# Performance work log

Hardware: AMD Instinct MI355X
Metric: run time of the kernel (lower is better)

Reference implementation:

```python
import jax, jax.numpy as jnp
import numpy as np

EPS = 1e-15

def gcn_sparse(x, row, col, ew, W, b, n):
    # PyG GCNConv: h = x@W; add self-loops (weight 1); sym-normalize; aggregate at col (target); + bias
    h = x @ W
    loop = jnp.arange(n)
    r = jnp.concatenate([row, loop])
    c = jnp.concatenate([col, loop])
    w = jnp.concatenate([ew, jnp.ones((n,), x.dtype)])
    deg = jax.ops.segment_sum(w, c, num_segments=n)
    dinv = jnp.where(deg > 0, deg ** -0.5, 0.0)
    norm = dinv[r] * w * dinv[c]
    out = jax.ops.segment_sum(norm[:, None] * h[r], c, num_segments=n)
    return out + b

def gcn_dense(x, adj, W, b):
    # Dense equivalent of dense_to_sparse + GCNConv: existing nonzero self-loops keep their
    # weight, zero-diagonal nodes get a self-loop of weight 1 (add_remaining_self_loops).
    diag = jnp.diagonal(adj)
    adj_h = adj + jnp.diag(jnp.where(diag == 0, 1.0, 0.0).astype(adj.dtype))
    deg = adj_h.sum(axis=0)  # degree at target (col) nodes
    dinv = jnp.where(deg > 0, deg ** -0.5, 0.0)
    a_norm = dinv[:, None] * adj_h * dinv[None, :]  # norm_ij = d_i^-1/2 a_ij d_j^-1/2
    return a_norm.T @ (x @ W) + b  # out_j = sum_i norm_ij h_i

def diff_pool(x, adj, s, mask=None):
    s = jax.nn.softmax(s, axis=-1)
    if mask is not None:
        x = x * mask[:, None]
        s = s * mask[:, None]
    out = s.T @ x                      # [C, F]
    out_adj = s.T @ (adj @ s)          # [C, C]
    link = jnp.linalg.norm(adj - s @ s.T) / adj.size
    ent = jnp.mean(jnp.sum(-s * jnp.log(s + EPS), axis=-1))
    return out, out_adj, link, ent

def setup_inputs() -> dict:
    N, E, F, H, C1, C2, NC = 8192, 262144, 128, 128, 1024, 128, 16
    key = jax.random.key(0)
    ks = jax.random.split(key, 16)
    x0 = jax.random.normal(ks[0], (N, F), dtype=jnp.float32)
    edge_index = jax.random.randint(ks[1], (2, E), 0, N, dtype=jnp.int32)
    edge_weight = jax.random.uniform(ks[2], (E,), dtype=jnp.float32)
    adj = jnp.zeros((N, N), jnp.float32).at[edge_index[0], edge_index[1]].add(edge_weight)
    mask = jnp.ones((N,), jnp.float32)
    g = lambda k, i, o: jax.random.normal(k, (i, o), dtype=jnp.float32) * (1.0 / np.sqrt(i))
    return {
        'x0': x0, 'edge_index': edge_index, 'edge_weight': edge_weight,
        'adj': adj, 'mask': mask,
        'W0_in': g(ks[3], F, H),      'b0_in': jnp.zeros((H,)),
        'Wp1':   g(ks[4], H, C1),     'bp1':   jnp.zeros((C1,)),
        'W1_in': g(ks[5], H, H),      'b1_in': jnp.zeros((H,)),
        'Wp2':   g(ks[6], H, C2),     'bp2':   jnp.zeros((C2,)),
        'W2_in': g(ks[7], H, H),      'b2_in': jnp.zeros((H,)),
        'W1_out': g(ks[8], 2 * H, H), 'b1_out': jnp.zeros((H,)),
        'W0_out': g(ks[9], 2 * H, NC), 'b0_out': jnp.zeros((NC,)),
    }

def reference(x0, edge_index, edge_weight, adj, mask,
              W0_in, b0_in, Wp1, bp1, W1_in, b1_in, Wp2, bp2,
              W2_in, b2_in, W1_out, b1_out, W0_out, b0_out):
    n = x0.shape[0]
    row, col = edge_index[0], edge_index[1]
    x0_ = jax.nn.relu(gcn_sparse(x0, row, col, edge_weight, W0_in, b0_in, n))
    s1 = jax.nn.relu(gcn_sparse(x0_, row, col, edge_weight, Wp1, bp1, n))
    x1, adj1, l1, e1 = diff_pool(x0_, adj, s1, mask)
    x1_ = jax.nn.relu(gcn_dense(x1, adj1, W1_in, b1_in))
    s2 = jax.nn.relu(gcn_dense(x1_, adj1, Wp2, bp2))
    x2, adj2, l2, e2 = diff_pool(x1_, adj1, s2)
    x2_out = jax.nn.relu(gcn_dense(x2, adj2, W2_in, b2_in))
    x2_out_up = s2 @ x2_out  # unpool with pre-softmax relu s2, as in source
    x1_out = jax.nn.relu(gcn_dense(jnp.concatenate([x1_, x2_out_up], axis=1), adj1, W1_out, b1_out))
    x1_out_up = s1 @ x1_out
    x0_out = jax.nn.relu(gcn_sparse(jnp.concatenate([x0_, x1_out_up], axis=1), row, col, edge_weight, W0_out, b0_out, n))
    prediction = jax.nn.log_softmax(x0_out, axis=1)
    edge_loss = l1 + e1 + l2 + e2
    return prediction, s1, edge_loss, adj1
```

## Files before the change

kernel.cpp:

```cpp
#include <hip/hip_runtime.h>
#include <math.h>


#define N_NODES 8192
#define N_EDGES 262144

typedef __attribute__((ext_vector_type(8))) short short8;
typedef __attribute__((ext_vector_type(4))) float floatx4;

#define OFF_DEG     0
#define OFF_CNTC    8192
#define OFF_CNTR    16384
#define OFF_SCAL    24576
#define ZERO_FLOATS 24592
#define OFF_COLPTR  24592
#define OFF_ROWPTR  32785
#define OFF_CURC    40978
#define OFF_CURR    49170
#define OFF_COLR    57362
#define OFF_COLN    319506
#define OFF_ROWC    581650
#define OFF_ROWW    843794
#define OFF_DINV    1105938
#define OFF_X0      1114144
#define OFF_H0      2162720
#define OFF_S       3211296
#define OFF_AN1TB   OFF_S
#define OFF_ADJ1B   (OFF_S+524288)
#define OFF_HAT     (OFF_S+1048576)
#define OFF_HBT     (OFF_S+1114112)
#define OFF_HCATT   (OFF_S+1179648)
#define OFF_S2ST    (OFF_S+1245184)
#define OFF_X0T     7405600
#define OFF_X0B     7929888
#define A2          8454176
#define OFF_X1      (A2+0)
#define OFF_Y16     (A2+131072)
#define OFF_X1_     (A2+262144)
#define OFF_S2      (A2+524288)
#define OFF_S2S     (A2+655360)
#define OFF_U       (A2+786432)
#define OFF_X2      (A2+917504)
#define OFF_ADJ2    (A2+933888)
#define OFF_HC      (A2+950272)
#define OFF_X2_     (A2+966656)
#define OFF_Z2      (A2+999424)
#define OFF_X1O     (A2+1261568)
#define OFF_P16     (A2+1392640)
#define OFF_DEG1    OFF_P16
#define OFF_DIAGV   (OFF_P16+1024)
#define OFF_DI2     (A2+1656832)
#define OFF_DF2     (A2+1656960)
#define OFF_ST      10111264
#define OFF_TBF     14305568
#define OFF_WP1T    OFF_TBF
#define OFF_PT      OFF_TBF
#define OFF_S1B     22694176
#define OFF_TT2     32131360

#define OUT_PRED 0
#define OUT_S1   131072
#define OUT_LOSS 8519680
#define OUT_ADJ1 8519681

__device__ __forceinline__ unsigned short f2bf(float f) {
    union { float f; unsigned u; } v; v.f = f;
    unsigned r = (v.u + 0x7FFF + ((v.u >> 16) & 1)) >> 16;
    return (unsigned short)r;
}
__device__ __forceinline__ float bf2f(unsigned short b) {
    union { unsigned u; float f; } v; v.u = (unsigned)b << 16; return v.f;
}
__device__ __forceinline__ void gl_lds16(const unsigned short* g, unsigned short* l) {
    __builtin_amdgcn_global_load_lds(
        (const __attribute__((address_space(1))) void*)g,
        (__attribute__((address_space(3))) void*)l, 16, 0, 0);
}


__global__ void k_hist(const int* __restrict__ row, const int* __restrict__ col,
                       const float* __restrict__ ew, int E,
                       float* deg, int* cntc, int* cntr, float* sumA2) {
    __shared__ float red[256];
    int e = blockIdx.x * 256 + threadIdx.x;
    float w2 = 0.f;
    if (e < E) {
        int r = row[e], c = col[e];
        float w = ew[e];
        atomicAdd(&deg[c], w);
        atomicAdd(&cntc[c], 1);
        atomicAdd(&cntr[r], 1);
        w2 = w * w;
    }
    red[threadIdx.x] = w2; __syncthreads();
    for (int s = 128; s > 0; s >>= 1) { if (threadIdx.x < s) red[threadIdx.x] += red[threadIdx.x + s]; __syncthreads(); }
    if (threadIdx.x == 0) atomicAdd(sumA2, red[0]);
}

__global__ __launch_bounds__(1024) void k_scan(const int* cntc, const int* cntr,
        int* colptr, int* rowptr, int* curc, int* curr, int n, int E,
        const float* __restrict__ deg, float* __restrict__ dinv) {
    __shared__ int part[1024];
    int tid = threadIdx.x;
    const int per = 8;
    for (int pass = 0; pass < 2; ++pass) {
        const int* cnt = pass ? cntr : cntc;
        int* ptr = pass ? rowptr : colptr;
        int* cur = pass ? curr : curc;
        int st = tid * per;
        int loc[per]; int s = 0;
        for (int i = 0; i < per; ++i) { loc[i] = s; s += cnt[st + i]; }
        part[tid] = s; __syncthreads();
        for (int off = 1; off < 1024; off <<= 1) {
            int v = part[tid];
            int add = (tid >= off) ? part[tid - off] : 0;
            __syncthreads();
            part[tid] = v + add;
            __syncthreads();
        }
// ... 3 lines not shown
        __syncthreads();
    }
    for (int i = tid; i < n; i += 1024) {
        float d = deg[i] + 1.0f;
        dinv[i] = (d > 0.f) ? 1.0f / sqrtf(d) : 0.f;
    }
}

__global__ void k_scatter(const int* __restrict__ row, const int* __restrict__ col,
                          const float* __restrict__ ew, int E, const float* __restrict__ dinv,
                          int* curc, int* curr, int* colr, float* coln, int* rowc, float* roww) {
    int e = blockIdx.x * 256 + threadIdx.x;
    if (e >= E) return;
    int r = row[e], c = col[e];
    float w = ew[e];
    float nrm = dinv[r] * w * dinv[c];
    int p = atomicAdd(&curc[c], 1);
    colr[p] = r; coln[p] = nrm;
    int q = atomicAdd(&curr[r], 1);
    rowc[q] = c; roww[q] = w;
}


__global__ __launch_bounds__(256) void gemm_ab_b16(const float* __restrict__ A, const float* __restrict__ B,
        unsigned short* __restrict__ C, int M, int N, int K) {
    __shared__ float As[16][68];
    __shared__ float Bs[16][68];
    int tid = threadIdx.x, tx = tid & 15, ty = tid >> 4;
    int m0 = blockIdx.y * 64, n0 = blockIdx.x * 64;
    float acc[4][4] = {};
    for (int k0 = 0; k0 < K; k0 += 16) {
        for (int l = 0; l < 4; ++l) {
            int idx = tid + 256 * l;
            int mm = idx >> 4, kk = idx & 15;
            As[kk][mm] = A[(size_t)(m0 + mm) * K + k0 + kk];
            int kk2 = idx >> 6, nn = idx & 63;
            Bs[kk2][nn] = B[(size_t)(k0 + kk2) * N + n0 + nn];
        }
        __syncthreads();
        #pragma unroll
        for (int kk = 0; kk < 16; ++kk) {
            float a[4], b[4];
            #pragma unroll
            for (int i = 0; i < 4; ++i) a[i] = As[kk][ty * 4 + i];
            #pragma unroll
            for (int j = 0; j < 4; ++j) b[j] = Bs[kk][tx * 4 + j];
            #pragma unroll
            for (int i = 0; i < 4; ++i)
                #pragma unroll
                for (int j = 0; j < 4; ++j) acc[i][j] += a[i] * b[j];
        }
        __syncthreads();
    }
    for (int i = 0; i < 4; ++i)
        for (int j = 0; j < 4; ++j)
            C[(size_t)(m0 + ty * 4 + i) * N + n0 + tx * 4 + j] = f2bf(acc[i][j]);
}

__global__ __launch_bounds__(256) void gemm_ab32(const float* __restrict__ A, const float* __restrict__ B,
        float* __restrict__ C, int M, int N, int K,
        const float* __restrict__ bias, int relu, int accum) {
    __shared__ float As[32][33];
    __shared__ float Bs[32][33];
    int tid = threadIdx.x, tx = tid & 15, ty = tid >> 4;
    int m0 = blockIdx.y * 32, n0 = blockIdx.x * 32;
    float acc[2][2] = {};
    for (int k0 = 0; k0 < K; k0 += 32) {
        #pragma unroll
        for (int l = 0; l < 4; ++l) {
            int idx = tid + 256 * l;
            int r = idx >> 5, c = idx & 31;
            As[r][c] = A[(size_t)(m0 + r) * K + k0 + c];
            Bs[r][c] = B[(size_t)(k0 + r) * N + n0 + c];
        }
        __syncthreads();
        #pragma unroll
        for (int kk = 0; kk < 32; ++kk) {
            float a0 = As[ty * 2][kk], a1 = As[ty * 2 + 1][kk];
            float b0 = Bs[kk][tx * 2], b1 = Bs[kk][tx * 2 + 1];
            acc[0][0] += a0 * b0; acc[0][1] += a0 * b1;
            acc[1][0] += a1 * b0; acc[1][1] += a1 * b1;
// ... 215 lines not shown
        #pragma unroll
        for (int i = 0; i < 2; ++i)
            #pragma unroll
            for (int j = 0; j < 2; ++j)
                hC[(size_t)(m0 + ty * 2 + i) * 128 + n0 + tx * 2 + j] = acc[i][j];
    } else {
        if (blockIdx.x | blockIdx.y) return;
        __shared__ float red[256];
        int tid = threadIdx.x;
        float diag = 0.f;
        if (tid < 128) {
            float s = 0.f;
            for (int i = 0; i < 128; ++i) s += adj2[(size_t)i * 128 + tid];
            diag = adj2[(size_t)tid * 128 + tid];
            float fix = (diag == 0.f) ? 1.0f : 0.f;
            s += fix;
            df2[tid] = fix;
            di2[tid] = (s > 0.f) ? 1.0f / sqrtf(s) : 0.f;
        }
        red[tid] = diag; __syncthreads();
        for (int st = 128; st > 0; st >>= 1) { if (tid < st) red[tid] += red[tid + st]; __syncthreads(); }
        if (tid == 0) *cross2_out = red[0];
    }
}

__global__ __launch_bounds__(256) void k_gemm_n16(const float* __restrict__ A, const float* __restrict__ B,
        float* __restrict__ C, int M, int K, int accum) {
    __shared__ float As[16][64];
    __shared__ float Bs[64][16];
    int tid = threadIdx.x;
    int r = tid >> 4, c = tid & 15;
    int m0 = blockIdx.x * 16;
    float acc = 0.f;
    for (int k0 = 0; k0 < K; k0 += 64) {
        #pragma unroll
        for (int l = 0; l < 4; ++l) {
            int idx = tid + 256 * l;
            int rr = idx >> 6, cc = idx & 63;
            As[rr][cc] = A[(size_t)(m0 + rr) * K + k0 + cc];
            int kk = idx >> 4, c2 = idx & 15;
            Bs[kk][c2] = B[(size_t)(k0 + kk) * 16 + c2];
        }
        __syncthreads();
        #pragma unroll 16
        for (int kk = 0; kk < 64; ++kk) acc += As[r][kk] * Bs[kk][c];
        __syncthreads();
    }
    float* p = &C[(size_t)(m0 + r) * 16 + c];
    if (accum) acc += *p;
    *p = acc;
}


__global__ __launch_bounds__(256) void gemm_tn_bf16_tiles(
        const unsigned short* __restrict__ ST_,
        const unsigned short* __restrict__ TT_,
        const unsigned short* __restrict__ X0T_,
        float* __restrict__ P, int K) {
    __shared__ __align__(16) unsigned short As[128 * 64];
    __shared__ __align__(16) unsigned short Bs[128 * 64];
    int tid = threadIdx.x;
    int wave = tid >> 6, lane = tid & 63;
    int wm = wave >> 1, wn = wave & 1;
    int lin = blockIdx.x + gridDim.x * blockIdx.y;
    int p432 = (lin & 7) * 54 + (lin >> 3);
    int f = p432 >> 2, z = p432 & 3;
    int m = 0, Pfx = 0;
    while (f >= Pfx + 17 - m) { Pfx += 17 - m; ++m; }
    int r = f - Pfx;
    int t, n0; const unsigned short* B;
    if (r < 8)           { t = m * 8 + r;                              n0 = r * 128;            B = TT_; }
    else if (r < 16 - m) { int tj = m + (r - 8);
                           t = 64 + (8 * m - m * (m - 1) / 2) + (r - 8); n0 = tj * 128;         B = ST_; }
    else                 { t = 100 + m;                                n0 = 0;                  B = X0T_; }
    int m0 = m * 128;
    int kchunk = K >> 2;
    int k0 = z * kchunk;
    float* Pz = P + ((size_t)z * 108 + t) * 16384;
    floatx4 acc[4][4] = {};
    int q = lane >> 4, lm = lane & 15;
    int lrow = lane >> 3, lcol = (lane & 7) * 8;
    for (int kt = 0; kt < kchunk; kt += 64) {
        int gk0 = k0 + kt;
        #pragma unroll
        for (int p = 0; p < 4; ++p) {
            int rbase = wave * 32 + p * 8;
            int row = rbase + lrow;
            int scol = lcol ^ ((row & 7) * 8);
            gl_lds16(&ST_[(size_t)(m0 + row) * K + gk0 + scol], &As[rbase * 64]);
            gl_lds16(&B[(size_t)(n0 + row) * K + gk0 + scol], &Bs[rbase * 64]);
        }
        __syncthreads();
        #pragma unroll
        for (int ks = 0; ks < 64; ks += 32) {
            short8 af[4], bf[4];
            int kk = ks + q * 8;
            #pragma unroll
            for (int i = 0; i < 4; ++i) {
                int ml = wm * 64 + i * 16 + lm;
                af[i] = *(const short8*)(&As[ml * 64 + (kk ^ ((ml & 7) * 8))]);
                int nl = wn * 64 + i * 16 + lm;
                bf[i] = *(const short8*)(&Bs[nl * 64 + (kk ^ ((nl & 7) * 8))]);
            }
            #pragma unroll
            for (int i = 0; i < 4; ++i)
                #pragma unroll
                for (int j = 0; j < 4; ++j)
                    acc[i][j] = __builtin_amdgcn_mfma_f32_16x16x32_bf16(af[i], bf[j], acc[i][j], 0, 0, 0);
        }
        __syncthreads();
    }
    for (int i = 0; i < 4; ++i) {
        int lr = wm * 64 + i * 16 + q * 4;
// ... 64 lines not shown
    if (kind == 0) {
        atomicAdd(&colsum[cc + 0], cs0);
        atomicAdd(&colsum[cc + 1], cs1);
        atomicAdd(&colsum[cc + 2], cs2);
        atomicAdd(&colsum[cc + 3], cs3);
    }
    __syncthreads();
    if (kind == 0 && tid < 128)
        atomicAdd(&deg1[n * 128 + tid], colsum[tid]);
    red[tid] = ss; __syncthreads();
    for (int s = 128; s > 0; s >>= 1) { if (tid < s) red[tid] += red[tid + s]; __syncthreads(); }
    if (tid == 0) atomicAdd((kind == 0) ? &scal[4] : &scal[2], red[0]);
    if (diagTile) {
        __syncthreads();
        red[tid] = tr; __syncthreads();
        for (int s = 128; s > 0; s >>= 1) { if (tid < s) red[tid] += red[tid + s]; __syncthreads(); }
        if (tid == 0) atomicAdd(&scal[1], red[0]);
    }
}

__global__ __launch_bounds__(256) void gemm_tn_bf16_n128(
        const unsigned short* __restrict__ A, const unsigned short* __restrict__ B,
        float* __restrict__ C, int K,
        const float* __restrict__ bias, int relu) {
    __shared__ __align__(16) unsigned short As[64 * 64];
    __shared__ __align__(16) unsigned short Bs[64 * 64];
    int tid = threadIdx.x, wave = tid >> 6, lane = tid & 63;
    int m0 = blockIdx.x * 64, n0 = blockIdx.y * 64;
    floatx4 acc[4] = {};
    int q = lane >> 4, lm = lane & 15;
    int lrow = lane >> 3, lcol = (lane & 7) * 8;
    for (int kt = 0; kt < K; kt += 64) {
        #pragma unroll
        for (int p = 0; p < 2; ++p) {
            int rbase = wave * 16 + p * 8;
            int row = rbase + lrow;
            int scol = lcol ^ ((row & 7) * 8);
            gl_lds16(&A[(size_t)(m0 + row) * K + kt + scol], &As[rbase * 64]);
            gl_lds16(&B[(size_t)(n0 + row) * K + kt + scol], &Bs[rbase * 64]);
        }
        __syncthreads();
        #pragma unroll
        for (int ks = 0; ks < 64; ks += 32) {
            int kk = ks + q * 8;
            int ml = wave * 16 + lm;
            short8 af = *(const short8*)(&As[ml * 64 + (kk ^ ((ml & 7) * 8))]);
            #pragma unroll
            for (int j = 0; j < 4; ++j) {
                int nl = j * 16 + lm;
                short8 bf = *(const short8*)(&Bs[nl * 64 + (kk ^ ((nl & 7) * 8))]);
                acc[j] = __builtin_amdgcn_mfma_f32_16x16x32_bf16(af, bf, acc[j], 0, 0, 0);
            }
        }
        __syncthreads();
    }
    #pragma unroll
    for (int j = 0; j < 4; ++j) {
        int col = n0 + j * 16 + lm;
        float bv = bias ? bias[col] : 0.f;
        int rowb = m0 + wave * 16 + q * 4;
        #pragma unroll
        for (int r = 0; r < 4; ++r) {
            float v = acc[j][r] + bv;
            if (relu) v = fmaxf(v, 0.f);
            C[(size_t)(rowb + r) * 128 + col] = v;
        }
    }
}

__global__ __launch_bounds__(256) void gemm_tn_bf16_store(
        const unsigned short* __restrict__ A, const unsigned short* __restrict__ B,
        float* __restrict__ C, unsigned short* __restrict__ Cb, int M, int N, int K,
        const float* __restrict__ bias, int relu) {
    __shared__ __align__(16) unsigned short As[128 * 64];
    __shared__ __align__(16) unsigned short Bs[128 * 64];
    int tid = threadIdx.x;
    int wave = tid >> 6, lane = tid & 63;
    int wm = wave >> 1, wn = wave & 1;
    int m0 = blockIdx.x * 128, n0 = blockIdx.y * 128;
    floatx4 acc[4][4] = {};
    int q = lane >> 4, lm = lane & 15;
    int lrow = lane >> 3, lcol = (lane & 7) * 8;
    for (int kt = 0; kt < K; kt += 64) {
        #pragma unroll
        for (int p = 0; p < 4; ++p) {
            int rbase = wave * 32 + p * 8;
            int row = rbase + lrow;
            int scol = lcol ^ ((row & 7) * 8);
            gl_lds16(&A[(size_t)(m0 + row) * K + kt + scol], &As[rbase * 64]);
// ... 69 lines not shown
            for (int ks = 0; ks < 64; ks += 32) {
                int kk = ks + q * 8;
                short8 bf = *(const short8*)(&Bs[lm * 64 + (kk ^ ((lm & 7) * 8))]);
                #pragma unroll
                for (int i = 0; i < 2; ++i) {
                    int ml = wave * 32 + i * 16 + lm;
                    short8 af = *(const short8*)(&As[ml * 64 + (kk ^ ((ml & 7) * 8))]);
                    acc[i] = __builtin_amdgcn_mfma_f32_16x16x32_bf16(af, bf, acc[i], 0, 0, 0);
                }
            }
            __syncthreads();
        }
    }
    #pragma unroll
    for (int i = 0; i < 2; ++i) {
        int rowb = m0 + wave * 32 + i * 16 + q * 4;
        #pragma unroll
        for (int r = 0; r < 4; ++r)
            C[(size_t)(rowb + r) * 16 + lm] = acc[i][r];
    }
}


__global__ __launch_bounds__(256) void k_transpose_f2b(
        const float* __restrict__ in, unsigned short* __restrict__ outb,
        int R, int C, const float* __restrict__ rowscale) {
    __shared__ float tile[64][65];
    int rb = blockIdx.y * 64, cb = blockIdx.x * 64;
    int t = threadIdx.x;
    int lr = t >> 4, lc4 = (t & 15) * 4;
    #pragma unroll
    for (int p = 0; p < 4; ++p) {
        int r = rb + lr + p * 16;
        float4 v = *(const float4*)(in + (size_t)r * C + cb + lc4);
        float s = rowscale ? rowscale[r] : 1.0f;
        tile[lr + p * 16][lc4 + 0] = v.x * s;
        tile[lr + p * 16][lc4 + 1] = v.y * s;
        tile[lr + p * 16][lc4 + 2] = v.z * s;
        tile[lr + p * 16][lc4 + 3] = v.w * s;
    }
    __syncthreads();
    int cc0 = t >> 5, rr = (t & 31) * 2;
    #pragma unroll
    for (int p = 0; p < 8; ++p) {
        int cc = cc0 + p * 8;
        unsigned a = f2bf(tile[rr][cc]);
        unsigned b = f2bf(tile[rr + 1][cc]);
        *(unsigned*)(outb + (size_t)(cb + cc) * R + rb + rr) = a | (b << 16);
    }
}

__global__ __launch_bounds__(256) void k_transpose_b2b2(
        const unsigned short* __restrict__ in0, unsigned short* __restrict__ out0,
        const unsigned short* __restrict__ in1, unsigned short* __restrict__ out1,
        int R, int C) {
    __shared__ __align__(16) unsigned short tile[64][72];
    const unsigned short* in = blockIdx.z ? in1 : in0;
    unsigned short* out = blockIdx.z ? out1 : out0;
    int rb = blockIdx.y * 64, cb = blockIdx.x * 64;
    int t = threadIdx.x;
    int lr = t >> 3, lc = (t & 7) * 8;
    #pragma unroll
    for (int p = 0; p < 2; ++p) {
        int r = lr + p * 32;
        *(short8*)(&tile[r][lc]) = *(const short8*)(&in[(size_t)(rb + r) * C + cb + lc]);
    }
    __syncthreads();
    int cc0 = t >> 4, rr = (t & 15) * 4;
    #pragma unroll
    for (int p = 0; p < 4; ++p) {
        int cc = cc0 + p * 16;
        unsigned long long v = (unsigned long long)tile[rr][cc]
                             | ((unsigned long long)tile[rr + 1][cc] << 16)
                             | ((unsigned long long)tile[rr + 2][cc] << 32)
                             | ((unsigned long long)tile[rr + 3][cc] << 48);
        *(unsigned long long*)(&out[(size_t)(cb + cc) * R + rb + rr]) = v;
    }
}

__global__ __launch_bounds__(256) void k_anorm_tb(const float* __restrict__ adjm, int n,
        const float* __restrict__ deg1, const float* __restrict__ diagv,
        unsigned short* __restrict__ outb) {
    __shared__ float tile[64][65];
    __shared__ float drow[64], frow[64], dcol[64];
    int rb = blockIdx.y * 64, cb = blockIdx.x * 64;
    int t = threadIdx.x;
    if (t < 64) {
        int i = rb + t;
        float fi = (diagv[i] == 0.f) ? 1.0f : 0.f;
        float s = deg1[i] + fi;
        frow[t] = fi;
        drow[t] = (s > 0.f) ? 1.0f / sqrtf(s) : 0.f;
    } else if (t < 128) {
        int j = cb + (t - 64);
        float fj = (diagv[j] == 0.f) ? 1.0f : 0.f;
        float s = deg1[j] + fj;
        dcol[t - 64] = (s > 0.f) ? 1.0f / sqrtf(s) : 0.f;
    }
    __syncthreads();
    int lr = t >> 4, lc4 = (t & 15) * 4;
    #pragma unroll
    for (int p = 0; p < 4; ++p) {
        int rl = lr + p * 16;
        int i = rb + rl;
        float4 v = *(const float4*)(adjm + (size_t)i * n + cb + lc4);
        float di = drow[rl];
        float vv[4] = {v.x, v.y, v.z, v.w};
        #pragma unroll
        for (int qq = 0; qq < 4; ++qq) {
            int j = cb + lc4 + qq;
            float val = vv[qq];
            if (i == j) val += frow[rl];
            tile[rl][lc4 + qq] = di * val * dcol[lc4 + qq];
        }
    }
    __syncthreads();
    int cc0 = t >> 5, rr = (t & 31) * 2;
    #pragma unroll
    for (int p = 0; p < 8; ++p) {
        int cc = cc0 + p * 8;
        unsigned a = f2bf(tile[rr][cc]);
        unsigned b = f2bf(tile[rr + 1][cc]);
        *(unsigned*)(outb + (size_t)(cb + cc) * n + rb + rr) = a | (b << 16);
    }
}


__global__ __launch_bounds__(64) void k_agg_b16(const unsigned short* __restrict__ h,
        float* __restrict__ out, unsigned short* __restrict__ outb,
        const int* __restrict__ cptr, const int* __restrict__ colr,
        const float* __restrict__ coln, const float* __restrict__ dinv,
        const float* __restrict__ bias, int relu) {
    int c = blockIdx.x, t = threadIdx.x;
    int f0 = t * 2;
    float d = dinv[c], dd = d * d;
    const unsigned short* hf = h + f0;
    unsigned u = *(const unsigned*)(hf + (size_t)c * 128);
    float a0 = dd * bf2f((unsigned short)(u & 0xffff));
    float a1 = dd * bf2f((unsigned short)(u >> 16));
    int e0 = cptr[c], e1 = cptr[c + 1];
    int e = e0;
    for (; e + 4 <= e1; e += 4) {
        int r0 = colr[e], r1 = colr[e + 1], r2 = colr[e + 2], r3 = colr[e + 3];
        float w0 = coln[e], w1 = coln[e + 1], w2 = coln[e + 2], w3 = coln[e + 3];
        unsigned v0 = *(const unsigned*)(hf + (size_t)r0 * 128);
        unsigned v1 = *(const unsigned*)(hf + (size_t)r1 * 128);
        unsigned v2 = *(const unsigned*)(hf + (size_t)r2 * 128);
// ... 102 lines not shown
    float v = xr[tid];
    red[tid] = v; __syncthreads();
    for (int s = 64; s > 0; s >>= 1) { if (tid < s) red[tid] = fmaxf(red[tid], red[tid + s]); __syncthreads(); }
    float m = red[0]; __syncthreads();
    float e = expf(v - m);
    red[tid] = e; __syncthreads();
    for (int s = 64; s > 0; s >>= 1) { if (tid < s) red[tid] += red[tid + s]; __syncthreads(); }
    float Z = red[0];
    float inv = 1.0f / Z, lz = logf(Z);
    __syncthreads();
    float sv = e * inv;
    S[(size_t)row * 128 + tid] = sv;
    STb[(size_t)tid * 1024 + row] = f2bf(sv);
    red[tid] = sv * (m + lz - v); __syncthreads();
    for (int s = 64; s > 0; s >>= 1) { if (tid < s) red[tid] += red[tid + s]; __syncthreads(); }
    if (tid == 0) atomicAdd(ent_acc, red[0]);
}

__global__ __launch_bounds__(256) void k_spmm_seg(const unsigned short* __restrict__ Sb,
        const int* __restrict__ rptr, const int* __restrict__ rowc, const float* __restrict__ roww,
        unsigned short* __restrict__ tb) {
    int wave = threadIdx.x >> 6, lane = threadIdx.x & 63;
    int r = blockIdx.x * 4 + wave;
    int j0 = blockIdx.y * 256 + lane * 4;
    const unsigned short* Sj = Sb + j0;
    float a0 = 0.f, a1 = 0.f, a2 = 0.f, a3 = 0.f;
    int e0 = rptr[r], e1 = rptr[r + 1];
    int e = e0;
    for (; e + 4 <= e1; e += 4) {
        int c0 = rowc[e], c1 = rowc[e + 1], c2 = rowc[e + 2], c3 = rowc[e + 3];
        float w0 = roww[e], w1 = roww[e + 1], w2 = roww[e + 2], w3 = roww[e + 3];
        uint2 v0 = *(const uint2*)(Sj + (size_t)c0 * 1024);
        uint2 v1 = *(const uint2*)(Sj + (size_t)c1 * 1024);
        uint2 v2 = *(const uint2*)(Sj + (size_t)c2 * 1024);
        uint2 v3 = *(const uint2*)(Sj + (size_t)c3 * 1024);
        a0 += w0 * bf2f((unsigned short)(v0.x & 0xffff)) + w1 * bf2f((unsigned short)(v1.x & 0xffff))
            + w2 * bf2f((unsigned short)(v2.x & 0xffff)) + w3 * bf2f((unsigned short)(v3.x & 0xffff));
        a1 += w0 * bf2f((unsigned short)(v0.x >> 16)) + w1 * bf2f((unsigned short)(v1.x >> 16))
            + w2 * bf2f((unsigned short)(v2.x >> 16)) + w3 * bf2f((unsigned short)(v3.x >> 16));
        a2 += w0 * bf2f((unsigned short)(v0.y & 0xffff)) + w1 * bf2f((unsigned short)(v1.y & 0xffff))
            + w2 * bf2f((unsigned short)(v2.y & 0xffff)) + w3 * bf2f((unsigned short)(v3.y & 0xffff));
        a3 += w0 * bf2f((unsigned short)(v0.y >> 16)) + w1 * bf2f((unsigned short)(v1.y >> 16))
            + w2 * bf2f((unsigned short)(v2.y >> 16)) + w3 * bf2f((unsigned short)(v3.y >> 16));
    }
    for (; e < e1; ++e) {
        int c = rowc[e]; float w = roww[e];
        uint2 v = *(const uint2*)(Sj + (size_t)c * 1024);
        a0 += w * bf2f((unsigned short)(v.x & 0xffff));
        a1 += w * bf2f((unsigned short)(v.x >> 16));
        a2 += w * bf2f((unsigned short)(v.y & 0xffff));
        a3 += w * bf2f((unsigned short)(v.y >> 16));
    }
    unsigned lo = (unsigned)f2bf(a0) | ((unsigned)f2bf(a1) << 16);
    unsigned hi = (unsigned)f2bf(a2) | ((unsigned)f2bf(a3) << 16);
    unsigned long long o = (unsigned long long)lo | ((unsigned long long)hi << 32);
    *(unsigned long long*)(tb + (size_t)r * 1024 + j0) = o;
}


extern "C" void kernel_launch(void* const* d_in, const int* in_sizes, int n_in,
                              void* d_out, int out_size, void* d_ws, size_t ws_size,
                              hipStream_t stream) {
    const int N = N_NODES, E = N_EDGES;
    const float* x0     = (const float*)d_in[0];
    const int*   eidx   = (const int*)d_in[1];
    const float* ew     = (const float*)d_in[2];
    const float* mask   = (const float*)d_in[4];
    const float* W0_in  = (const float*)d_in[5];
    const float* b0_in  = (const float*)d_in[6];
    const float* Wp1    = (const float*)d_in[7];
    const float* bp1    = (const float*)d_in[8];
    const float* W1_in  = (const float*)d_in[9];
    const float* b1_in  = (const float*)d_in[10];
    const float* Wp2    = (const float*)d_in[11];
    const float* bp2    = (const float*)d_in[12];
    const float* W2_in  = (const float*)d_in[13];
    const float* b2_in  = (const float*)d_in[14];
    const float* W1_out = (const float*)d_in[15];
    const float* b1_out = (const float*)d_in[16];
// ... 29 lines not shown
    unsigned short* ADJ1B = (unsigned short*)(wsf + OFF_ADJ1B);
    unsigned short* HAT   = (unsigned short*)(wsf + OFF_HAT);
    unsigned short* HBT   = (unsigned short*)(wsf + OFF_HBT);
    unsigned short* HCATT = (unsigned short*)(wsf + OFF_HCATT);
    unsigned short* S2ST  = (unsigned short*)(wsf + OFF_S2ST);
    unsigned short* ST    = (unsigned short*)(wsf + OFF_ST);
    unsigned short* TBF   = (unsigned short*)(wsf + OFF_TBF);
    unsigned short* WP1T  = (unsigned short*)(wsf + OFF_WP1T);
    unsigned short* X0T   = (unsigned short*)(wsf + OFF_X0T);
    unsigned short* x0b   = (unsigned short*)(wsf + OFF_X0B);
    unsigned short* s1b   = (unsigned short*)(wsf + OFF_S1B);
    float* PT    = wsf + OFF_PT;
    float* x1    = wsf + OFF_X1;
    float* y16   = wsf + OFF_Y16;
    float* x1_   = wsf + OFF_X1_;
    float* s2    = wsf + OFF_S2;
    float* S2s   = wsf + OFF_S2S;
    float* u     = wsf + OFF_U;
    float* x2    = wsf + OFF_X2;
    float* adj2  = wsf + OFF_ADJ2;
    float* hC    = wsf + OFF_HC;
    float* x2_   = wsf + OFF_X2_;
    float* z2    = wsf + OFF_Z2;
    float* x1o_  = wsf + OFF_X1O;
    float* p16   = wsf + OFF_P16;
    float* deg1  = wsf + OFF_DEG1;
    float* diagv = wsf + OFF_DIAGV;
    float* di2   = wsf + OFF_DI2;
    float* df2   = wsf + OFF_DF2;

    const int* row = eidx;
    const int* col = eidx + E;

    hipMemsetAsync(wsf, 0, (size_t)ZERO_FLOATS * sizeof(float), stream);
    hipMemsetAsync(deg1, 0, 1024 * sizeof(float), stream);

    k_hist<<<E / 256, 256, 0, stream>>>(row, col, ew, E, deg, cntc, cntr, &scal[3]);
    k_scan<<<1, 1024, 0, stream>>>(cntc, cntr, cptr, rptr, curc, curr, N, E, deg, dinv);
    k_scatter<<<E / 256, 256, 0, stream>>>(row, col, ew, E, dinv, curc, curr, colr, coln, rowc, roww);

    gemm_ab_b16<<<dim3(2, 128), 256, 0, stream>>>(x0, W0_in, h0b, 8192, 128, 128);
    k_agg_b16<<<N, 64, 0, stream>>>(h0b, x0_, x0b, cptr, colr, coln, dinv, b0_in, 1);

    k_agg_b16<<<N, 64, 0, stream>>>(x0b, nullptr, h0b, cptr, colr, coln, dinv, nullptr, 0);
    k_transpose_f2b<<<dim3(16, 2), 256, 0, stream>>>(Wp1, WP1T, 128, 1024, nullptr);
    gemm_tn_bf16_store<<<dim3(64, 8), 256, 0, stream>>>(h0b, WP1T, s1o, s1b, 8192, 1024, 128, bp1, 1);

    k_softmax1024<<<N, 256, 0, stream>>>(s1o, Sb, mask, &scal[0]);
    k_spmm_seg<<<dim3(N / 4, 4), 256, 0, stream>>>(Sb, rptr, rowc, roww, TBF);
    k_transpose_b2b2<<<dim3(16, 128, 2), 256, 0, stream>>>(Sb, ST, TBF, TT, 8192, 1024);
    k_transpose_f2b<<<dim3(2, 128), 256, 0, stream>>>(x0_, X0T, 8192, 128, mask);

    gemm_tn_bf16_tiles<<<dim3(108, 4), 256, 0, stream>>>(ST, TT, X0T, PT, 8192);
    k_reduce_tiles<<<dim3(2, 108), 256, 0, stream>>>(PT, adj1o, ADJ1B, x1, deg1, diagv, scal);
    k_anorm_tb<<<dim3(16, 16), 256, 0, stream>>>(adj1o, 1024, deg1, diagv, AN1TB);

    gemm_ab32_bt<<<dim3(4, 32), 256, 0, stream>>>(x1, W1_in, HAT, 1024, 128, 128);
    gemm_tn_bf16_n128<<<dim3(16, 2), 256, 0, stream>>>(AN1TB, HAT, x1_, 1024, b1_in, 1);
    gemm_ab32_bt<<<dim3(4, 32), 256, 0, stream>>>(x1_, Wp2, HBT, 1024, 128, 128);
    gemm_tn_bf16_n128<<<dim3(16, 2), 256, 0, stream>>>(AN1TB, HBT, s2, 1024, bp2, 1);

    k_softmax128_t<<<1024, 128, 0, stream>>>(s2, S2s, S2ST, &scal[5]);
    gemm_tn_bf16_n128<<<dim3(16, 2), 256, 0, stream>>>(ADJ1B, S2ST, u, 1024, nullptr, 0);
    k_atb32_3<<<dim3(4, 4, 3), 256, 0, stream>>>(S2s, x1_, u, S2s, x2, adj2, &scal[7], 128, 128, 1024);

    k_hC_coldfix<<<dim3(4, 4, 2), 256, 0, stream>>>(x2, W2_in, hC, adj2, di2, df2, &scal[6]);
    gemm_atb32n<<<dim3(4, 4), 256, 0, stream>>>(adj2, hC, x2_, 128, 128, 128, b2_in, di2, df2, di2);

    gemm_ab32<<<dim3(4, 4), 256, 0, stream>>>(x2_, W1_out + 128 * 128, z2, 128, 128, 128, nullptr, 0, 0);
    gemm_dual_bt<<<dim3(4, 32), 256, 0, stream>>>(x1_, W1_out, s2, z2, HCATT, 1024, 128, 128);
    gemm_tn_bf16_n128<<<dim3(16, 2), 256, 0, stream>>>(AN1TB, HCATT, x1o_, 1024, b1_out, 1);

    k_gemm_n16<<<64, 256, 0, stream>>>(x1o_, W0_out + 128 * 16, y16, 1024, 128, 0);
    k_gemm16_mfma<<<64, 256, 0, stream>>>(x0b, s1b, W0_out, y16, p16);
    k_agg16_ls<<<512, 256, 0, stream>>>(p16, predo, cptr, colr, coln, dinv, b0_out, scal, losso);
}
```

Baseline: 883.9 us.

## Merge independent small kernels and fuse the x1_out projection into its GEMM epilogue

```diff
diff --git a/kernel.cpp b/kernel.cpp
--- a/kernel.cpp
+++ b/kernel.cpp
@@ -45,7 +45,6 @@
 #define OFF_HC      (A2+950272)
 #define OFF_X2_     (A2+966656)
 #define OFF_Z2      (A2+999424)
-#define OFF_X1O     (A2+1261568)
 #define OFF_P16     (A2+1392640)
 #define OFF_DEG1    OFF_P16
 #define OFF_DIAGV   (OFF_P16+1024)
@@ -78,23 +77,64 @@
 }
 
 
-__global__ void k_hist(const int* __restrict__ row, const int* __restrict__ col,
-                       const float* __restrict__ ew, int E,
-                       float* deg, int* cntc, int* cntr, float* sumA2) {
-    __shared__ float red[256];
-    int e = blockIdx.x * 256 + threadIdx.x;
-    float w2 = 0.f;
-    if (e < E) {
-        int r = row[e], c = col[e];
-        float w = ew[e];
-        atomicAdd(&deg[c], w);
-        atomicAdd(&cntc[c], 1);
-        atomicAdd(&cntr[r], 1);
-        w2 = w * w;
-    }
-    red[threadIdx.x] = w2; __syncthreads();
-    for (int s = 128; s > 0; s >>= 1) { if (threadIdx.x < s) red[threadIdx.x] += red[threadIdx.x + s]; __syncthreads(); }
-    if (threadIdx.x == 0) atomicAdd(sumA2, red[0]);
+__global__ __launch_bounds__(256) void k_hist_gemm(
+        const int* __restrict__ row, const int* __restrict__ col,
+        const float* __restrict__ ew, int E,
+        float* deg, int* cntc, int* cntr, float* sumA2,
+        const float* __restrict__ A, const float* __restrict__ B,
+        unsigned short* __restrict__ C) {
+    __shared__ float As[16][68];
+    __shared__ float Bs[16][68];
+    int tid = threadIdx.x;
+    if (blockIdx.x < 1024) {
+        float* red = &As[0][0];
+        int e = blockIdx.x * 256 + tid;
+        float w2 = 0.f;
+        if (e < E) {
+            int r = row[e], c = col[e];
+            float w = ew[e];
+            atomicAdd(&deg[c], w);
+            atomicAdd(&cntc[c], 1);
+            atomicAdd(&cntr[r], 1);
+            w2 = w * w;
+        }
+        red[tid] = w2; __syncthreads();
+        for (int s = 128; s > 0; s >>= 1) { if (tid < s) red[tid] += red[tid + s]; __syncthreads(); }
+        if (tid == 0) atomicAdd(sumA2, red[0]);
+        return;
+    }
+    int bidx = blockIdx.x - 1024;
+    int tx = tid & 15, ty = tid >> 4;
+    int m0 = (bidx >> 1) * 64, n0 = (bidx & 1) * 64;
+    const int M = 8192, N = 128, K = 128;
+    float acc[4][4] = {};
+    for (int k0 = 0; k0 < K; k0 += 16) {
+        for (int l = 0; l < 4; ++l) {
+            int idx = tid + 256 * l;
+            int mm = idx >> 4, kk = idx & 15;
+            As[kk][mm] = A[(size_t)(m0 + mm) * K + k0 + kk];
+            int kk2 = idx >> 6, nn = idx & 63;
+            Bs[kk2][nn] = B[(size_t)(k0 + kk2) * N + n0 + nn];
+        }
+        __syncthreads();
+        #pragma unroll
+        for (int kk = 0; kk < 16; ++kk) {
+            float a[4], b[4];
+            #pragma unroll
+            for (int i = 0; i < 4; ++i) a[i] = As[kk][ty * 4 + i];
+            #pragma unroll
+            for (int j = 0; j < 4; ++j) b[j] = Bs[kk][tx * 4 + j];
+            #pragma unroll
+            for (int i = 0; i < 4; ++i)
+                #pragma unroll
+                for (int j = 0; j < 4; ++j) acc[i][j] += a[i] * b[j];
+        }
+        __syncthreads();
+    }
+    for (int i = 0; i < 4; ++i)
+        for (int j = 0; j < 4; ++j)
+            C[(size_t)(m0 + ty * 4 + i) * N + n0 + tx * 4 + j] = f2bf(acc[i][j]);
+    (void)M;
 }
 
 __global__ __launch_bounds__(1024) void k_scan(const int* cntc, const int* cntr,
@@ -144,41 +184,6 @@
 }
 
 
-__global__ __launch_bounds__(256) void gemm_ab_b16(const float* __restrict__ A, const float* __restrict__ B,
-        unsigned short* __restrict__ C, int M, int N, int K) {
-    __shared__ float As[16][68];
-    __shared__ float Bs[16][68];
-    int tid = threadIdx.x, tx = tid & 15, ty = tid >> 4;
-    int m0 = blockIdx.y * 64, n0 = blockIdx.x * 64;
-    float acc[4][4] = {};
-    for (int k0 = 0; k0 < K; k0 += 16) {
-        for (int l = 0; l < 4; ++l) {
-            int idx = tid + 256 * l;
-            int mm = idx >> 4, kk = idx & 15;
-            As[kk][mm] = A[(size_t)(m0 + mm) * K + k0 + kk];
-            int kk2 = idx >> 6, nn = idx & 63;
-            Bs[kk2][nn] = B[(size_t)(k0 + kk2) * N + n0 + nn];
-        }
-        __syncthreads();
-        #pragma unroll
-        for (int kk = 0; kk < 16; ++kk) {
-            float a[4], b[4];
-            #pragma unroll
-            for (int i = 0; i < 4; ++i) a[i] = As[kk][ty * 4 + i];
-            #pragma unroll
-            for (int j = 0; j < 4; ++j) b[j] = Bs[kk][tx * 4 + j];
-            #pragma unroll
-            for (int i = 0; i < 4; ++i)
-                #pragma unroll
-                for (int j = 0; j < 4; ++j) acc[i][j] += a[i] * b[j];
-        }
-        __syncthreads();
-    }
-    for (int i = 0; i < 4; ++i)
-        for (int j = 0; j < 4; ++j)
-            C[(size_t)(m0 + ty * 4 + i) * N + n0 + tx * 4 + j] = f2bf(acc[i][j]);
-}
-
 __global__ __launch_bounds__(256) void gemm_ab32(const float* __restrict__ A, const float* __restrict__ B,
         float* __restrict__ C, int M, int N, int K,
         const float* __restrict__ bias, int relu, int accum) {
@@ -440,33 +445,6 @@
         for (int st = 128; st > 0; st >>= 1) { if (tid < st) red[tid] += red[tid + st]; __syncthreads(); }
         if (tid == 0) *cross2_out = red[0];
     }
-}
-
-__global__ __launch_bounds__(256) void k_gemm_n16(const float* __restrict__ A, const float* __restrict__ B,
-        float* __restrict__ C, int M, int K, int accum) {
-    __shared__ float As[16][64];
-    __shared__ float Bs[64][16];
-    int tid = threadIdx.x;
-    int r = tid >> 4, c = tid & 15;
-    int m0 = blockIdx.x * 16;
-    float acc = 0.f;
-    for (int k0 = 0; k0 < K; k0 += 64) {
-        #pragma unroll
-        for (int l = 0; l < 4; ++l) {
-            int idx = tid + 256 * l;
-            int rr = idx >> 6, cc = idx & 63;
-            As[rr][cc] = A[(size_t)(m0 + rr) * K + k0 + cc];
-            int kk = idx >> 4, c2 = idx & 15;
-            Bs[kk][c2] = B[(size_t)(k0 + kk) * 16 + c2];
-        }
-        __syncthreads();
-        #pragma unroll 16
-        for (int kk = 0; kk < 64; ++kk) acc += As[r][kk] * Bs[kk][c];
-        __syncthreads();
-    }
-    float* p = &C[(size_t)(m0 + r) * 16 + c];
-    if (accum) acc += *p;
-    *p = acc;
 }
 
 
@@ -487,10 +465,10 @@
     while (f >= Pfx + 17 - m) { Pfx += 17 - m; ++m; }
     int r = f - Pfx;
     int t, n0; const unsigned short* B;
-    if (r < 8)           { t = m * 8 + r;                              n0 = r * 128;            B = TT_; }
+    if (r < 8)           { t = m * 8 + r;                                n0 = r * 128;    B = TT_; }
     else if (r < 16 - m) { int tj = m + (r - 8);
-                           t = 64 + (8 * m - m * (m - 1) / 2) + (r - 8); n0 = tj * 128;         B = ST_; }
-    else                 { t = 100 + m;                                n0 = 0;                  B = X0T_; }
+                           t = 64 + (8 * m - m * (m - 1) / 2) + (r - 8); n0 = tj * 128;   B = ST_; }
+    else                 { t = 100 + m;                                  n0 = 0;          B = X0T_; }
     int m0 = m * 128;
     int kchunk = K >> 2;
     int k0 = z * kchunk;
@@ -503,10 +481,10 @@
         #pragma unroll
         for (int p = 0; p < 4; ++p) {
             int rbase = wave * 32 + p * 8;
-            int row = rbase + lrow;
-            int scol = lcol ^ ((row & 7) * 8);
-            gl_lds16(&ST_[(size_t)(m0 + row) * K + gk0 + scol], &As[rbase * 64]);
-            gl_lds16(&B[(size_t)(n0 + row) * K + gk0 + scol], &Bs[rbase * 64]);
+            int rrow = rbase + lrow;
+            int scol = lcol ^ ((rrow & 7) * 8);
+            gl_lds16(&ST_[(size_t)(m0 + rrow) * K + gk0 + scol], &As[rbase * 64]);
+            gl_lds16(&B[(size_t)(n0 + rrow) * K + gk0 + scol], &Bs[rbase * 64]);
         }
         __syncthreads();
         #pragma unroll
@@ -617,9 +595,11 @@
 __global__ __launch_bounds__(256) void gemm_tn_bf16_n128(
         const unsigned short* __restrict__ A, const unsigned short* __restrict__ B,
         float* __restrict__ C, int K,
-        const float* __restrict__ bias, int relu) {
+        const float* __restrict__ bias, int relu,
+        const float* __restrict__ Wy, float* __restrict__ y16acc) {
     __shared__ __align__(16) unsigned short As[64 * 64];
     __shared__ __align__(16) unsigned short Bs[64 * 64];
+    __shared__ float Cs[64 * 65];
     int tid = threadIdx.x, wave = tid >> 6, lane = tid & 63;
     int m0 = blockIdx.x * 64, n0 = blockIdx.y * 64;
     floatx4 acc[4] = {};
@@ -651,15 +631,32 @@
     }
     #pragma unroll
     for (int j = 0; j < 4; ++j) {
-        int col = n0 + j * 16 + lm;
+        int lc = j * 16 + lm;
+        int col = n0 + lc;
         float bv = bias ? bias[col] : 0.f;
-        int rowb = m0 + wave * 16 + q * 4;
+        int lrb = wave * 16 + q * 4;
         #pragma unroll
         for (int r = 0; r < 4; ++r) {
             float v = acc[j][r] + bv;
             if (relu) v = fmaxf(v, 0.f);
-            C[(size_t)(rowb + r) * 128 + col] = v;
-        }
+            if (C) C[(size_t)(m0 + lrb + r) * 128 + col] = v;
+            if (Wy) Cs[(lrb + r) * 65 + lc] = v;
+        }
+    }
+    if (!Wy) return;
+    float* Wys = (float*)Bs;
+    for (int e = tid; e < 1024; e += 256)
+        Wys[e] = Wy[(size_t)(n0 + (e >> 4)) * 16 + (e & 15)];
+    __syncthreads();
+    #pragma unroll
+    for (int k4 = 0; k4 < 4; ++k4) {
+        int oidx = tid * 4 + k4;
+        int orow = oidx >> 4, ocol = oidx & 15;
+        float val = 0.f;
+        #pragma unroll 16
+        for (int j = 0; j < 64; ++j)
+            val += Cs[orow * 65 + j] * Wys[j * 16 + ocol];
+        atomicAdd(&y16acc[(size_t)(m0 + orow) * 16 + ocol], val);
     }
 }
 
@@ -775,32 +772,40 @@
 }
 
 
-__global__ __launch_bounds__(256) void k_transpose_f2b(
+__device__ __forceinline__ void f2b_body(float* tile ,
         const float* __restrict__ in, unsigned short* __restrict__ outb,
-        int R, int C, const float* __restrict__ rowscale) {
-    __shared__ float tile[64][65];
-    int rb = blockIdx.y * 64, cb = blockIdx.x * 64;
-    int t = threadIdx.x;
+        int R, int C, const float* __restrict__ rowscale, int bx, int by, int t) {
+    int rb = by * 64, cb = bx * 64;
     int lr = t >> 4, lc4 = (t & 15) * 4;
     #pragma unroll
     for (int p = 0; p < 4; ++p) {
         int r = rb + lr + p * 16;
         float4 v = *(const float4*)(in + (size_t)r * C + cb + lc4);
         float s = rowscale ? rowscale[r] : 1.0f;
-        tile[lr + p * 16][lc4 + 0] = v.x * s;
-        tile[lr + p * 16][lc4 + 1] = v.y * s;
-        tile[lr + p * 16][lc4 + 2] = v.z * s;
-        tile[lr + p * 16][lc4 + 3] = v.w * s;
+        tile[(lr + p * 16) * 65 + lc4 + 0] = v.x * s;
+        tile[(lr + p * 16) * 65 + lc4 + 1] = v.y * s;
+        tile[(lr + p * 16) * 65 + lc4 + 2] = v.z * s;
+        tile[(lr + p * 16) * 65 + lc4 + 3] = v.w * s;
     }
     __syncthreads();
     int cc0 = t >> 5, rr = (t & 31) * 2;
     #pragma unroll
     for (int p = 0; p < 8; ++p) {
         int cc = cc0 + p * 8;
-        unsigned a = f2bf(tile[rr][cc]);
-        unsigned b = f2bf(tile[rr + 1][cc]);
+        unsigned a = f2bf(tile[rr * 65 + cc]);
+        unsigned b = f2bf(tile[(rr + 1) * 65 + cc]);
         *(unsigned*)(outb + (size_t)(cb + cc) * R + rb + rr) = a | (b << 16);
     }
+}
+
+__global__ __launch_bounds__(256) void k_f2b2(
+        const float* __restrict__ in0, unsigned short* __restrict__ out0,
+        const float* __restrict__ in1, unsigned short* __restrict__ out1,
+        const float* __restrict__ mask) {
+    __shared__ float tile[64 * 65];
+    int b = blockIdx.x, t = threadIdx.x;
+    if (b < 32) f2b_body(tile, in0, out0, 128, 1024, nullptr, b & 15, b >> 4, t);
+    else { int bb = b - 32; f2b_body(tile, in1, out1, 8192, 128, mask, bb & 1, bb >> 1, t); }
 }
 
 __global__ __launch_bounds__(256) void k_transpose_b2b2(
@@ -831,51 +836,98 @@
     }
 }
 
-__global__ __launch_bounds__(256) void k_anorm_tb(const float* __restrict__ adjm, int n,
+__global__ __launch_bounds__(256) void k_anorm_hat(const float* __restrict__ adjm,
         const float* __restrict__ deg1, const float* __restrict__ diagv,
-        unsigned short* __restrict__ outb) {
-    __shared__ float tile[64][65];
-    __shared__ float drow[64], frow[64], dcol[64];
-    int rb = blockIdx.y * 64, cb = blockIdx.x * 64;
+        unsigned short* __restrict__ outb,
+        const float* __restrict__ Ax1, const float* __restrict__ BW1,
+        unsigned short* __restrict__ HATo) {
+    __shared__ float sm[64 * 65 + 192];
     int t = threadIdx.x;
-    if (t < 64) {
-        int i = rb + t;
-        float fi = (diagv[i] == 0.f) ? 1.0f : 0.f;
-        float s = deg1[i] + fi;
-        frow[t] = fi;
-        drow[t] = (s > 0.f) ? 1.0f / sqrtf(s) : 0.f;
-    } else if (t < 128) {
-        int j = cb + (t - 64);
-        float fj = (diagv[j] == 0.f) ? 1.0f : 0.f;
-        float s = deg1[j] + fj;
-        dcol[t - 64] = (s > 0.f) ? 1.0f / sqrtf(s) : 0.f;
-    }
+    if (blockIdx.x < 256) {
+        const int n = 1024;
+        float* tile = sm;
+        float* drow = sm + 4160;
+        float* frow = sm + 4224;
+        float* dcol = sm + 4288;
+        int rb = (blockIdx.x >> 4) * 64, cb = (blockIdx.x & 15) * 64;
+        if (t < 64) {
+            int i = rb + t;
+            float fi = (diagv[i] == 0.f) ? 1.0f : 0.f;
+            float s = deg1[i] + fi;
+            frow[t] = fi;
+            drow[t] = (s > 0.f) ? 1.0f / sqrtf(s) : 0.f;
+        } else if (t < 128) {
+            int j = cb + (t - 64);
+            float fj = (diagv[j] == 0.f) ? 1.0f : 0.f;
+            float s = deg1[j] + fj;
+            dcol[t - 64] = (s > 0.f) ? 1.0f / sqrtf(s) : 0.f;
+        }
+        __syncthreads();
+        int lr = t >> 4, lc4 = (t & 15) * 4;
+        #pragma unroll
+        for (int p = 0; p < 4; ++p) {
+            int rl = lr + p * 16;
+            int i = rb + rl;
+            float4 v = *(const float4*)(adjm + (size_t)i * n + cb + lc4);
+            float di = drow[rl];
+            float vv[4] = {v.x, v.y, v.z, v.w};
+            #pragma unroll
+            for (int qq = 0; qq < 4; ++qq) {
+                int j = cb + lc4 + qq;
+                float val = vv[qq];
+                if (i == j) val += frow[rl];
+                tile[rl * 65 + lc4 + qq] = di * val * dcol[lc4 + qq];
+            }
+        }
+        __syncthreads();
+        int cc0 = t >> 5, rr = (t & 31) * 2;
+        #pragma unroll
+        for (int p = 0; p < 8; ++p) {
+            int cc = cc0 + p * 8;
+            unsigned a = f2bf(tile[rr * 65 + cc]);
+            unsigned b = f2bf(tile[(rr + 1) * 65 + cc]);
+            *(unsigned*)(outb + (size_t)(cb + cc) * n + rb + rr) = a | (b << 16);
+        }
+        return;
+    }
+    int bb = blockIdx.x - 256;
+    float* As = sm;
+    float* Bs = sm + 1056;
+    int tx = t & 15, ty = t >> 4;
+    int m0 = (bb >> 2) * 32, n0 = (bb & 3) * 32;
+    const int M = 1024, N = 128, K = 128;
+    float acc[2][2] = {};
+    for (int k0 = 0; k0 < K; k0 += 32) {
+        #pragma unroll
+        for (int l = 0; l < 4; ++l) {
+            int idx = t + 256 * l;
+            int r = idx >> 5, c = idx & 31;
+            As[r * 33 + c] = Ax1[(size_t)(m0 + r) * K + k0 + c];
+            Bs[r * 33 + c] = BW1[(size_t)(k0 + r) * N + n0 + c];
+        }
+        __syncthreads();
+        #pragma unroll
+        for (int kk = 0; kk < 32; ++kk) {
+            float a0 = As[(ty * 2) * 33 + kk], a1 = As[(ty * 2 + 1) * 33 + kk];
+            float b0 = Bs[kk * 33 + tx * 2], b1 = Bs[kk * 33 + tx * 2 + 1];
+            acc[0][0] += a0 * b0; acc[0][1] += a0 * b1;
+            acc[1][0] += a1 * b0; acc[1][1] += a1 * b1;
+        }
+        __syncthreads();
+    }
+    #pragma unroll
+    for (int i = 0; i < 2; ++i)
+        #pragma unroll
+        for (int j = 0; j < 2; ++j)
+            As[(ty * 2 + i) * 33 + tx * 2 + j] = acc[i][j];
     __syncthreads();
-    int lr = t >> 4, lc4 = (t & 15) * 4;
-    #pragma unroll
-    for (int p = 0; p < 4; ++p) {
-        int rl = lr + p * 16;
-        int i = rb + rl;
-        float4 v = *(const float4*)(adjm + (size_t)i * n + cb + lc4);
-        float di = drow[rl];
-        float vv[4] = {v.x, v.y, v.z, v.w};
-        #pragma unroll
-        for (int qq = 0; qq < 4; ++qq) {
-            int j = cb + lc4 + qq;
-            float val = vv[qq];
-            if (i == j) val += frow[rl];
-            tile[rl][lc4 + qq] = di * val * dcol[lc4 + qq];
-        }
-    }
-    __syncthreads();
-    int cc0 = t >> 5, rr = (t & 31) * 2;
-    #pragma unroll
-    for (int p = 0; p < 8; ++p) {
-        int cc = cc0 + p * 8;
-        unsigned a = f2bf(tile[rr][cc]);
-        unsigned b = f2bf(tile[rr + 1][cc]);
-        *(unsigned*)(outb + (size_t)(cb + cc) * n + rb + rr) = a | (b << 16);
-    }
+    int nl = t >> 3, moff = (t & 7) * 4;
+    ushort4 o;
+    o.x = f2bf(As[(moff + 0) * 33 + nl]);
+    o.y = f2bf(As[(moff + 1) * 33 + nl]);
+    o.z = f2bf(As[(moff + 2) * 33 + nl]);
+    o.w = f2bf(As[(moff + 3) * 33 + nl]);
+    *(ushort4*)(HATo + (size_t)(n0 + nl) * M + m0 + moff) = o;
 }
 
 
@@ -1024,39 +1076,29 @@
         unsigned short* __restrict__ tb) {
     int wave = threadIdx.x >> 6, lane = threadIdx.x & 63;
     int r = blockIdx.x * 4 + wave;
-    int j0 = blockIdx.y * 256 + lane * 4;
+    int j0 = lane * 16;
     const unsigned short* Sj = Sb + j0;
-    float a0 = 0.f, a1 = 0.f, a2 = 0.f, a3 = 0.f;
+    float a[16] = {};
     int e0 = rptr[r], e1 = rptr[r + 1];
-    int e = e0;
-    for (; e + 4 <= e1; e += 4) {
-        int c0 = rowc[e], c1 = rowc[e + 1], c2 = rowc[e + 2], c3 = rowc[e + 3];
-        float w0 = roww[e], w1 = roww[e + 1], w2 = roww[e + 2], w3 = roww[e + 3];
-        uint2 v0 = *(const uint2*)(Sj + (size_t)c0 * 1024);
-        uint2 v1 = *(const uint2*)(Sj + (size_t)c1 * 1024);
-        uint2 v2 = *(const uint2*)(Sj + (size_t)c2 * 1024);
-        uint2 v3 = *(const uint2*)(Sj + (size_t)c3 * 1024);
-        a0 += w0 * bf2f((unsigned short)(v0.x & 0xffff)) + w1 * bf2f((unsigned short)(v1.x & 0xffff))
-            + w2 * bf2f((unsigned short)(v2.x & 0xffff)) + w3 * bf2f((unsigned short)(v3.x & 0xffff));
-        a1 += w0 * bf2f((unsigned short)(v0.x >> 16)) + w1 * bf2f((unsigned short)(v1.x >> 16))
-            + w2 * bf2f((unsigned short)(v2.x >> 16)) + w3 * bf2f((unsigned short)(v3.x >> 16));
-        a2 += w0 * bf2f((unsigned short)(v0.y & 0xffff)) + w1 * bf2f((unsigned short)(v1.y & 0xffff))
-            + w2 * bf2f((unsigned short)(v2.y & 0xffff)) + w3 * bf2f((unsigned short)(v3.y & 0xffff));
-        a3 += w0 * bf2f((unsigned short)(v0.y >> 16)) + w1 * bf2f((unsigned short)(v1.y >> 16))
-            + w2 * bf2f((unsigned short)(v2.y >> 16)) + w3 * bf2f((unsigned short)(v3.y >> 16));
-    }
-    for (; e < e1; ++e) {
+    for (int e = e0; e < e1; ++e) {
         int c = rowc[e]; float w = roww[e];
-        uint2 v = *(const uint2*)(Sj + (size_t)c * 1024);
-        a0 += w * bf2f((unsigned short)(v.x & 0xffff));
-        a1 += w * bf2f((unsigned short)(v.x >> 16));
-        a2 += w * bf2f((unsigned short)(v.y & 0xffff));
-        a3 += w * bf2f((unsigned short)(v.y >> 16));
-    }
-    unsigned lo = (unsigned)f2bf(a0) | ((unsigned)f2bf(a1) << 16);
-    unsigned hi = (unsigned)f2bf(a2) | ((unsigned)f2bf(a3) << 16);
-    unsigned long long o = (unsigned long long)lo | ((unsigned long long)hi << 32);
-    *(unsigned long long*)(tb + (size_t)r * 1024 + j0) = o;
+        const unsigned short* p = Sj + (size_t)c * 1024;
+        uint4 v0 = *(const uint4*)(p);
+        uint4 v1 = *(const uint4*)(p + 8);
+        unsigned vv[8] = {v0.x, v0.y, v0.z, v0.w, v1.x, v1.y, v1.z, v1.w};
+        #pragma unroll
+        for (int q = 0; q < 8; ++q) {
+            a[q * 2]     += w * bf2f((unsigned short)(vv[q] & 0xffff));
+            a[q * 2 + 1] += w * bf2f((unsigned short)(vv[q] >> 16));
+        }
+    }
+    unsigned ow[8];
+    #pragma unroll
+    for (int q = 0; q < 8; ++q)
+        ow[q] = (unsigned)f2bf(a[q * 2]) | ((unsigned)f2bf(a[q * 2 + 1]) << 16);
+    uint4* outp = (uint4*)(tb + (size_t)r * 1024 + j0);
+    outp[0] = make_uint4(ow[0], ow[1], ow[2], ow[3]);
+    outp[1] = make_uint4(ow[4], ow[5], ow[6], ow[7]);
 }
 
 
@@ -1132,7 +1174,6 @@
     float* hC    = wsf + OFF_HC;
     float* x2_   = wsf + OFF_X2_;
     float* z2    = wsf + OFF_Z2;
-    float* x1o_  = wsf + OFF_X1O;
     float* p16   = wsf + OFF_P16;
     float* deg1  = wsf + OFF_DEG1;
     float* diagv = wsf + OFF_DIAGV;
@@ -1144,34 +1185,33 @@
 
     hipMemsetAsync(wsf, 0, (size_t)ZERO_FLOATS * sizeof(float), stream);
     hipMemsetAsync(deg1, 0, 1024 * sizeof(float), stream);
-
-    k_hist<<<E / 256, 256, 0, stream>>>(row, col, ew, E, deg, cntc, cntr, &scal[3]);
+    hipMemsetAsync(y16, 0, 1024 * 16 * sizeof(float), stream);
+
+    k_hist_gemm<<<1280, 256, 0, stream>>>(row, col, ew, E, deg, cntc, cntr, &scal[3],
+                                          x0, W0_in, h0b);
     k_scan<<<1, 1024, 0, stream>>>(cntc, cntr, cptr, rptr, curc, curr, N, E, deg, dinv);
     k_scatter<<<E / 256, 256, 0, stream>>>(row, col, ew, E, dinv, curc, curr, colr, coln, rowc, roww);
 
-    gemm_ab_b16<<<dim3(2, 128), 256, 0, stream>>>(x0, W0_in, h0b, 8192, 128, 128);
     k_agg_b16<<<N, 64, 0, stream>>>(h0b, x0_, x0b, cptr, colr, coln, dinv, b0_in, 1);
 
     k_agg_b16<<<N, 64, 0, stream>>>(x0b, nullptr, h0b, cptr, colr, coln, dinv, nullptr, 0);
-    k_transpose_f2b<<<dim3(16, 2), 256, 0, stream>>>(Wp1, WP1T, 128, 1024, nullptr);
+    k_f2b2<<<288, 256, 0, stream>>>(Wp1, WP1T, x0_, X0T, mask);
     gemm_tn_bf16_store<<<dim3(64, 8), 256, 0, stream>>>(h0b, WP1T, s1o, s1b, 8192, 1024, 128, bp1, 1);
 
     k_softmax1024<<<N, 256, 0, stream>>>(s1o, Sb, mask, &scal[0]);
-    k_spmm_seg<<<dim3(N / 4, 4), 256, 0, stream>>>(Sb, rptr, rowc, roww, TBF);
+    k_spmm_seg<<<N / 4, 256, 0, stream>>>(Sb, rptr, rowc, roww, TBF);
     k_transpose_b2b2<<<dim3(16, 128, 2), 256, 0, stream>>>(Sb, ST, TBF, TT, 8192, 1024);
-    k_transpose_f2b<<<dim3(2, 128), 256, 0, stream>>>(x0_, X0T, 8192, 128, mask);
 
     gemm_tn_bf16_tiles<<<dim3(108, 4), 256, 0, stream>>>(ST, TT, X0T, PT, 8192);
     k_reduce_tiles<<<dim3(2, 108), 256, 0, stream>>>(PT, adj1o, ADJ1B, x1, deg1, diagv, scal);
-    k_anorm_tb<<<dim3(16, 16), 256, 0, stream>>>(adj1o, 1024, deg1, diagv, AN1TB);
-
-    gemm_ab32_bt<<<dim3(4, 32), 256, 0, stream>>>(x1, W1_in, HAT, 1024, 128, 128);
-    gemm_tn_bf16_n128<<<dim3(16, 2), 256, 0, stream>>>(AN1TB, HAT, x1_, 1024, b1_in, 1);
+    k_anorm_hat<<<384, 256, 0, stream>>>(adj1o, deg1, diagv, AN1TB, x1, W1_in, HAT);
+
+    gemm_tn_bf16_n128<<<dim3(16, 2), 256, 0, stream>>>(AN1TB, HAT, x1_, 1024, b1_in, 1, nullptr, nullptr);
     gemm_ab32_bt<<<dim3(4, 32), 256, 0, stream>>>(x1_, Wp2, HBT, 1024, 128, 128);
-    gemm_tn_bf16_n128<<<dim3(16, 2), 256, 0, stream>>>(AN1TB, HBT, s2, 1024, bp2, 1);
+    gemm_tn_bf16_n128<<<dim3(16, 2), 256, 0, stream>>>(AN1TB, HBT, s2, 1024, bp2, 1, nullptr, nullptr);
 
     k_softmax128_t<<<1024, 128, 0, stream>>>(s2, S2s, S2ST, &scal[5]);
-    gemm_tn_bf16_n128<<<dim3(16, 2), 256, 0, stream>>>(ADJ1B, S2ST, u, 1024, nullptr, 0);
+    gemm_tn_bf16_n128<<<dim3(16, 2), 256, 0, stream>>>(ADJ1B, S2ST, u, 1024, nullptr, 0, nullptr, nullptr);
     k_atb32_3<<<dim3(4, 4, 3), 256, 0, stream>>>(S2s, x1_, u, S2s, x2, adj2, &scal[7], 128, 128, 1024);
 
     k_hC_coldfix<<<dim3(4, 4, 2), 256, 0, stream>>>(x2, W2_in, hC, adj2, di2, df2, &scal[6]);
@@ -1179,9 +1219,9 @@
 
     gemm_ab32<<<dim3(4, 4), 256, 0, stream>>>(x2_, W1_out + 128 * 128, z2, 128, 128, 128, nullptr, 0, 0);
     gemm_dual_bt<<<dim3(4, 32), 256, 0, stream>>>(x1_, W1_out, s2, z2, HCATT, 1024, 128, 128);
-    gemm_tn_bf16_n128<<<dim3(16, 2), 256, 0, stream>>>(AN1TB, HCATT, x1o_, 1024, b1_out, 1);
-
-    k_gemm_n16<<<64, 256, 0, stream>>>(x1o_, W0_out + 128 * 16, y16, 1024, 128, 0);
+    gemm_tn_bf16_n128<<<dim3(16, 2), 256, 0, stream>>>(AN1TB, HCATT, nullptr, 1024, b1_out, 1,
+                                                       W0_out + 128 * 16, y16);
+
     k_gemm16_mfma<<<64, 256, 0, stream>>>(x0b, s1b, W0_out, y16, p16);
     k_agg16_ls<<<512, 256, 0, stream>>>(p16, predo, cptr, colr, coln, dinv, b0_out, scal, losso);
 }
```

New measurement: 889.1 us. About the same (+0.6%).
